# Performance work log

Hardware: AMD Instinct MI355X
Metric: run time of the kernel (lower is better)

## Reference

```python
import jax, jax.numpy as jnp
import numpy as np

N = 50000      # nodes
E = 800000     # edges (before self loops)
IN, H, OUT = 128, 64, 64
NEG_SLOPE = 0.2  # PyG GATConv leaky_relu slope


def _glorot(k, shape):
    lim = float(np.sqrt(6.0 / (shape[0] + shape[1])))
    return jax.random.uniform(k, shape, jnp.float32, -lim, lim)


def setup_inputs() -> dict:
    key = jax.random.key(0)
    ks = jax.random.split(key, 16)
    x = jax.random.normal(ks[0], (N, IN), jnp.float32)
    edge_src = jax.random.randint(ks[1], (E,), 0, N, jnp.int32)
    edge_dst = jax.random.randint(ks[2], (E,), 0, N, jnp.int32)
    dims = [(IN, H), (H, H), (H, OUT)]
    inp = {"x": x, "edge_src": edge_src, "edge_dst": edge_dst}
    i = 3
    for l, (di, do) in enumerate(dims):
        inp[f"W{l}"] = _glorot(ks[i], (di, do)); i += 1
        inp[f"as{l}"] = _glorot(ks[i], (1, do))[0]; i += 1
        inp[f"ad{l}"] = _glorot(ks[i], (1, do))[0]; i += 1
        inp[f"b{l}"] = jnp.zeros((do,), jnp.float32)
    return inp


def _gat_layer(x, W, a_src, a_dst, b, src, dst):
    # single-head GATConv (PyG semantics, self loops already in src/dst)
    h = x @ W                              # [N, do]
    s = h @ a_src                          # [N] source attention logits
    d = h @ a_dst                          # [N] dest attention logits
    e = jax.nn.leaky_relu(s[src] + d[dst], NEG_SLOPE)   # [E']
    # segment softmax over incoming edges of each destination node
    m = jax.ops.segment_max(e, dst, num_segments=N)
    w = jnp.exp(e - m[dst])
    denom = jax.ops.segment_sum(w, dst, num_segments=N)
    coef = w / (denom[dst] + 1e-16)
    out = jax.ops.segment_sum(h[src] * coef[:, None], dst, num_segments=N)
    return out + b


def reference(x, edge_src, edge_dst, W0, as0, ad0, b0, W1, as1, ad1, b1, W2, as2, ad2, b2):
    # add self loops (GATConv default add_self_loops=True)
    loop = jnp.arange(N, dtype=edge_src.dtype)
    src = jnp.concatenate([edge_src, loop])
    dst = jnp.concatenate([edge_dst, loop])
    h = jax.nn.relu(_gat_layer(x, W0, as0, ad0, b0, src, dst))
    # dropout is identity in eval mode
    h = jax.nn.relu(_gat_layer(h, W1, as1, ad1, b1, src, dst))
    return _gat_layer(h, W2, as2, ad2, b2, src, dst)
```

## Files before the change

### kernel.cpp

```cpp
#include <hip/hip_runtime.h>
#include <hip/hip_fp16.h>
#include <math.h>

#define WAVE 64
#define NEG_SLOPE 0.2f
#define BCAP 4096
#define CSTR (BCAP + 128)

typedef _Float16 half8 __attribute__((ext_vector_type(8)));
typedef float f32x4 __attribute__((ext_vector_type(4)));


template <int K, int IS_HALF>
__device__ __forceinline__ void gemm_body(
    char* smemRaw, int t, int bid,
    const void* __restrict__ Xv, const float* __restrict__ W,
    const float* __restrict__ a_s, const float* __restrict__ a_d,
    __half* __restrict__ H, float* __restrict__ S, float* __restrict__ D,
    int n) {
    constexpr int AK = K + 8;
    _Float16* Xs = (_Float16*)smemRaw;
    _Float16* Bt = Xs + 64 * AK;
    int base = bid * 64;

    {
        int row = t >> 2, q = t & 3;
        int grow = base + row;
        constexpr int CW = K / 4;
        if constexpr (IS_HALF) {
            const __half* Xh = (const __half*)Xv;
#pragma unroll
            for (int c0 = 0; c0 < CW; c0 += 8) {
                uint4 v = make_uint4(0, 0, 0, 0);
                if (grow < n) v = *(const uint4*)(Xh + (size_t)grow * K + q * CW + c0);
                *(uint4*)(Xs + row * AK + q * CW + c0) = v;
            }
        } else {
            const float* X = (const float*)Xv;
#pragma unroll
            for (int c0 = 0; c0 < CW; c0 += 8) {
                float4 v0 = make_float4(0.f, 0.f, 0.f, 0.f), v1 = v0;
                if (grow < n) {
                    v0 = *(const float4*)(X + (size_t)grow * K + q * CW + c0);
                    v1 = *(const float4*)(X + (size_t)grow * K + q * CW + c0 + 4);
                }
                _Float16 h[8] = {(_Float16)v0.x, (_Float16)v0.y, (_Float16)v0.z, (_Float16)v0.w,
                                 (_Float16)v1.x, (_Float16)v1.y, (_Float16)v1.z, (_Float16)v1.w};
                *(uint4*)(Xs + row * AK + q * CW + c0) = *(uint4*)h;
            }
        }
    }
    {
        int nn = t & 63, g = t >> 6;
        constexpr int KW = K / 4;
        _Float16 hbuf[KW];
#pragma unroll
        for (int j = 0; j < KW; ++j)
            hbuf[j] = (_Float16)W[(size_t)(g * KW + j) * 64 + nn];
#pragma unroll
        for (int j = 0; j < KW; j += 8)
            *(uint4*)(Bt + nn * AK + g * KW + j) = *(uint4*)(hbuf + j);
    }
    __syncthreads();

    int lane = t & 63;
    int wv = t >> 6;
    int m0 = wv * 16;
    int l15 = lane & 15, quad = lane >> 4;

    f32x4 acc[4] = {{0.f, 0.f, 0.f, 0.f}, {0.f, 0.f, 0.f, 0.f},
                    {0.f, 0.f, 0.f, 0.f}, {0.f, 0.f, 0.f, 0.f}};
#pragma unroll
    for (int ks = 0; ks < K; ks += 32) {
        half8 a = *(half8*)(Xs + (m0 + l15) * AK + ks + quad * 8);
#pragma unroll
        for (int cg = 0; cg < 4; ++cg) {
            half8 b = *(half8*)(Bt + (cg * 16 + l15) * AK + ks + quad * 8);
            acc[cg] = __builtin_amdgcn_mfma_f32_16x16x32_f16(a, b, acc[cg], 0, 0, 0);
        }
    }

    float as_c[4], ad_c[4];
#pragma unroll
    for (int cg = 0; cg < 4; ++cg) {
        as_c[cg] = a_s[cg * 16 + l15];
        ad_c[cg] = a_d[cg * 16 + l15];
    }
#pragma unroll
    for (int r = 0; r < 4; ++r) {
        int grow = base + m0 + quad * 4 + r;
        bool ok = grow < n;
        float ps = 0.f, pd = 0.f;
#pragma unroll
        for (int cg = 0; cg < 4; ++cg) {
            float v = acc[cg][r];
            if (ok) H[(size_t)grow * 64 + cg * 16 + l15] = __float2half(v);
            ps += v * as_c[cg];
            pd += v * ad_c[cg];
        }
        for (int o = 1; o < 16; o <<= 1) {
            ps += __shfl_xor(ps, o);
            pd += __shfl_xor(pd, o);
        }
        if (l15 == 0 && ok) { S[grow] = ps; D[grow] = pd; }
    }
}

__global__ __launch_bounds__(256) void place_gemm0_kernel(
    const int* __restrict__ src, const int* __restrict__ dst,
    int* __restrict__ gfill, int* __restrict__ binned, int e, int nb, int nchunk,
    const float* __restrict__ X, const float* __restrict__ W,
    const float* __restrict__ a_s, const float* __restrict__ a_d,
    __half* __restrict__ H, float* __restrict__ S, float* __restrict__ D, int n) {
    extern __shared__ char smem[];
    if ((int)blockIdx.x >= nchunk) {
        gemm_body<128, 0>(smem, threadIdx.x, blockIdx.x - nchunk,
                          X, W, a_s, a_d, H, S, D, n);
        return;
    }
    int* cnt = (int*)smem;
    int* bas = cnt + nb;
    for (int b = threadIdx.x; b < nb; b += 256) cnt[b] = 0;
    __syncthreads();
    int base = blockIdx.x * 4096;
#pragma unroll
    for (int k = 0; k < 16; ++k) {
        int i = base + k * 256 + threadIdx.x;
        if (i < e) atomicAdd(&cnt[dst[i] >> 7], 1);
    }
    __syncthreads();
    for (int b = threadIdx.x; b < nb; b += 256) {
        int c = cnt[b];
        bas[b] = c ? atomicAdd(&gfill[b], c) : 0;
        cnt[b] = 0;
    }
    __syncthreads();
#pragma unroll
    for (int k = 0; k < 16; ++k) {
        int i = base + k * 256 + threadIdx.x;
        if (i < e) {
            int d = dst[i];
            int bk = d >> 7;
            int r = atomicAdd(&cnt[bk], 1);
            binned[(size_t)bk * BCAP + bas[bk] + r] = ((d & 127) << 16) | src[i];
        }
    }
}

__global__ __launch_bounds__(256) void bucket_build_kernel(
    const int* __restrict__ binned, const int* __restrict__ gfill,
    int* __restrict__ csr_src, int2* __restrict__ rowse, int n) {
    __shared__ int cnt[128], off[128], pcnt[128];
    int b = blockIdx.x;
    int t = threadIdx.x;
    int nodeBase = b << 7;
    int nc = min(128, n - nodeBase);
    int ne = min(gfill[b], BCAP);
    const int* bp = binned + (size_t)b * BCAP;
    if (t < 128) { cnt[t] = 1; pcnt[t] = 1; }
    __syncthreads();
    for (int i = t; i < ne; i += 256)
        atomicAdd(&cnt[bp[i] >> 16], 1);
    __syncthreads();
    if (t < 128) off[t] = cnt[t];
    __syncthreads();
    for (int o = 1; o < 128; o <<= 1) {
        int u = (t >= o && t < 128) ? off[t - o] : 0;
        __syncthreads();
        if (t < 128) off[t] += u;
        __syncthreads();
    }
    if (t < 128) off[t] -= cnt[t];
    __syncthreads();
    int csrBase = b * CSTR;
    if (t < nc) {
        int st = csrBase + off[t];
        rowse[nodeBase + t] = make_int2(st, st + cnt[t]);
        csr_src[st] = nodeBase + t;
    }
    for (int i = t; i < ne; i += 256) {
        int p = bp[i];
        int loc = p >> 16;
        int r = atomicAdd(&pcnt[loc], 1);
        csr_src[csrBase + off[loc] + r] = p & 0xFFFF;
    }
}

template <int K, int IS_HALF>
__global__ __launch_bounds__(256) void mfma_gemm_feat_kernel(
    const void* __restrict__ Xv, const float* __restrict__ W,
    const float* __restrict__ a_s, const float* __restrict__ a_d,
    __half* __restrict__ H, float* __restrict__ S, float* __restrict__ D, int n) {
    __shared__ char smem[2 * 64 * (K + 8) * 2];
    gemm_body<K, IS_HALF>(smem, threadIdx.x, blockIdx.x, Xv, W, a_s, a_d, H, S, D, n);
}


template <int WRITE_HALF>
__global__ __launch_bounds__(256) void gat_aggregate_kernel(
    const __half* __restrict__ H, const float* __restrict__ S,
    const float* __restrict__ D, const int2* __restrict__ rowse,
    const int* __restrict__ csr_src, const float* __restrict__ bias,
    void* __restrict__ OUTp, int n, int do_relu) {
    int wid  = (blockIdx.x * blockDim.x + threadIdx.x) >> 6;
    int lane = threadIdx.x & 63;
    if (wid >= n) return;
    int eg = lane >> 3;
    int cg = lane & 7;
    int2 se = rowse[wid];
    int start = se.x, end = se.y;
    float d_i = D[wid];

    float z = 0.f;
    float acc[8] = {0.f, 0.f, 0.f, 0.f, 0.f, 0.f, 0.f, 0.f};

    for (int cb = start; cb < end; cb += WAVE) {
        int j = cb + lane;
        bool v = j < end;
        int sc = v ? csr_src[j] : 0;
        float sv = S[sc];
        float e = sv + d_i;
        e = (e > 0.f) ? e : NEG_SLOPE * e;
        float w = v ? __expf(e) : 0.f;
        z += w;

        int nch = min(WAVE, end - cb);
        int rounds = (nch + 7) >> 3;
#pragma unroll 4
        for (int r = 0; r < rounds; ++r) {
            int idx = 8 * r + eg;
            float wr = __shfl(w, idx);
            int   sr = __shfl(sc, idx);
            if (idx < nch) {
                uint4 u = *(const uint4*)(H + (size_t)sr * 64 + 8 * cg);
                float2 f0 = __half22float2(*(__half2*)&u.x);
                float2 f1 = __half22float2(*(__half2*)&u.y);
                float2 f2 = __half22float2(*(__half2*)&u.z);
                float2 f3 = __half22float2(*(__half2*)&u.w);
                acc[0] = fmaf(wr, f0.x, acc[0]);
                acc[1] = fmaf(wr, f0.y, acc[1]);
                acc[2] = fmaf(wr, f1.x, acc[2]);
                acc[3] = fmaf(wr, f1.y, acc[3]);
                acc[4] = fmaf(wr, f2.x, acc[4]);
                acc[5] = fmaf(wr, f2.y, acc[5]);
                acc[6] = fmaf(wr, f3.x, acc[6]);
                acc[7] = fmaf(wr, f3.y, acc[7]);
            }
        }
    }

    z += __shfl_xor(z, 1);
    z += __shfl_xor(z, 2);
    z += __shfl_xor(z, 4);
    for (int o = 8; o < 64; o <<= 1) {
#pragma unroll
        for (int jj = 0; jj < 8; ++jj) acc[jj] += __shfl_xor(acc[jj], o);
        z += __shfl_xor(z, o);
    }

    if (eg == 0) {
        float inv = 1.f / (z + 1e-16f);
        const float4 bv0 = *(const float4*)(bias + 8 * cg);
        const float4 bv1 = *(const float4*)(bias + 8 * cg + 4);
        float o[8];
        o[0] = acc[0] * inv + bv0.x;
        o[1] = acc[1] * inv + bv0.y;
        o[2] = acc[2] * inv + bv0.z;
        o[3] = acc[3] * inv + bv0.w;
        o[4] = acc[4] * inv + bv1.x;
        o[5] = acc[5] * inv + bv1.y;
        o[6] = acc[6] * inv + bv1.z;
        o[7] = acc[7] * inv + bv1.w;
        if (do_relu) {
#pragma unroll
            for (int jj = 0; jj < 8; ++jj) o[jj] = fmaxf(o[jj], 0.f);
        }
        if constexpr (WRITE_HALF) {
            _Float16 h[8];
#pragma unroll
            for (int jj = 0; jj < 8; ++jj) h[jj] = (_Float16)o[jj];
            *(uint4*)((__half*)OUTp + (size_t)wid * 64 + 8 * cg) = *(uint4*)h;
        } else {
            float* OUT = (float*)OUTp;
            *(float4*)(OUT + (size_t)wid * 64 + 8 * cg) = make_float4(o[0], o[1], o[2], o[3]);
            *(float4*)(OUT + (size_t)wid * 64 + 8 * cg + 4) = make_float4(o[4], o[5], o[6], o[7]);
        }
    }
}


static inline size_t align256(size_t x) { return (x + 255) & ~(size_t)255; }

extern "C" void kernel_launch(void* const* d_in, const int* in_sizes, int n_in,
                              void* d_out, int out_size, void* d_ws, size_t ws_size,
                              hipStream_t stream) {
    const float* x    = (const float*)d_in[0];
    const int*   esrc = (const int*)d_in[1];
    const int*   edst = (const int*)d_in[2];
    const int E = in_sizes[1];
    const int N = in_sizes[0] / 128;

    const float* W0 = (const float*)d_in[3];
    const float* as0 = (const float*)d_in[4];
    const float* ad0 = (const float*)d_in[5];
    const float* b0 = (const float*)d_in[6];
    const float* W1 = (const float*)d_in[7];
    const float* as1 = (const float*)d_in[8];
    const float* ad1 = (const float*)d_in[9];
    const float* b1 = (const float*)d_in[10];
    const float* W2 = (const float*)d_in[11];
    const float* as2 = (const float*)d_in[12];
    const float* ad2 = (const float*)d_in[13];
    const float* b2 = (const float*)d_in[14];

    const int NB = (N + 127) >> 7;

    char* p = (char*)d_ws;
    int*  gfill   = (int*)p;  p += align256((size_t)(NB + 1) * 4);
    int2* rowse   = (int2*)p; p += align256((size_t)N * 8);
    int*  csr_src = (int*)p;  p += align256((size_t)NB * CSTR * 4);
    int*  binned  = (int*)p;  p += align256((size_t)NB * BCAP * 4);
    __half* h16 = (__half*)p; p += align256((size_t)N * 64 * 2);
    __half* hA  = (__half*)p; p += align256((size_t)N * 64 * 2);
    __half* hB  = (__half*)p; p += align256((size_t)N * 64 * 2);
    float* sA = (float*)p; p += align256((size_t)N * 4);
    float* dA = (float*)p; p += align256((size_t)N * 4);
    float* out = (float*)d_out;

    int nchunk = (E + 4095) / 4096;
    int tile_grid = (N + 63) / 64;
    int agg_grid  = (N + 3) / 4;

    hipMemsetAsync(gfill, 0, (size_t)(NB + 1) * 4, stream);

    place_gemm0_kernel<<<nchunk + tile_grid, 256, 34816, stream>>>(
        esrc, edst, gfill, binned, E, NB, nchunk,
        x, W0, as0, ad0, h16, sA, dA, N);

    bucket_build_kernel<<<NB, 256, 0, stream>>>(binned, gfill, csr_src, rowse, N);

    gat_aggregate_kernel<1><<<agg_grid, 256, 0, stream>>>(
        h16, sA, dA, rowse, csr_src, b0, hA, N, 1);

    mfma_gemm_feat_kernel<64, 1><<<tile_grid, 256, 0, stream>>>(hA, W1, as1, ad1, h16, sA, dA, N);
    gat_aggregate_kernel<1><<<agg_grid, 256, 0, stream>>>(
        h16, sA, dA, rowse, csr_src, b1, hB, N, 1);

    mfma_gemm_feat_kernel<64, 1><<<tile_grid, 256, 0, stream>>>(hB, W2, as2, ad2, h16, sA, dA, N);
    gat_aggregate_kernel<0><<<agg_grid, 256, 0, stream>>>(
        h16, sA, dA, rowse, csr_src, b2, out, N, 0);
}
```

Measured before the change: 235.0 us.

## Split feature matrix into two 32-column halves and aggregate per half-wave

Stores the fp16 node features as two planar halves of 32 columns each. The aggregation now uses two waves per node, each gathering 64-byte rows from one half, and each edge-group lane computes its own attention weight directly instead of broadcasting weights and indices by shuffle. The aim is more waves in flight and smaller gather footprints for the irregular neighbor reads. In exchange, the attention logits, csr index and S lookups are computed twice per edge (once per half), and separate S/D buffers are added for the middle layer.

```diff
diff --git a/kernel.cpp b/kernel.cpp
--- a/kernel.cpp
+++ b/kernel.cpp
@@ -14,7 +14,8 @@
 template <int K, int IS_HALF>
 __device__ __forceinline__ void gemm_body(
     char* smemRaw, int t, int bid,
-    const void* __restrict__ Xv, const float* __restrict__ W,
+    const void* __restrict__ Xv, size_t HS,
+    const float* __restrict__ W,
     const float* __restrict__ a_s, const float* __restrict__ a_d,
     __half* __restrict__ H, float* __restrict__ S, float* __restrict__ D,
     int n) {
@@ -32,7 +33,9 @@
 #pragma unroll
             for (int c0 = 0; c0 < CW; c0 += 8) {
                 uint4 v = make_uint4(0, 0, 0, 0);
-                if (grow < n) v = *(const uint4*)(Xh + (size_t)grow * K + q * CW + c0);
+                if (grow < n)
+                    v = *(const uint4*)(Xh + (size_t)(q >> 1) * HS +
+                                        (size_t)grow * 32 + (q & 1) * 16 + c0);
                 *(uint4*)(Xs + row * AK + q * CW + c0) = v;
             }
         } else {
@@ -94,7 +97,8 @@
 #pragma unroll
         for (int cg = 0; cg < 4; ++cg) {
             float v = acc[cg][r];
-            if (ok) H[(size_t)grow * 64 + cg * 16 + l15] = __float2half(v);
+            if (ok) H[(size_t)(cg >> 1) * HS + (size_t)grow * 32 + (cg & 1) * 16 + l15] =
+                        __float2half(v);
             ps += v * as_c[cg];
             pd += v * ad_c[cg];
         }
@@ -109,13 +113,13 @@
 __global__ __launch_bounds__(256) void place_gemm0_kernel(
     const int* __restrict__ src, const int* __restrict__ dst,
     int* __restrict__ gfill, int* __restrict__ binned, int e, int nb, int nchunk,
-    const float* __restrict__ X, const float* __restrict__ W,
+    const float* __restrict__ X, size_t HS, const float* __restrict__ W,
     const float* __restrict__ a_s, const float* __restrict__ a_d,
     __half* __restrict__ H, float* __restrict__ S, float* __restrict__ D, int n) {
     extern __shared__ char smem[];
     if ((int)blockIdx.x >= nchunk) {
         gemm_body<128, 0>(smem, threadIdx.x, blockIdx.x - nchunk,
-                          X, W, a_s, a_d, H, S, D, n);
+                          X, HS, W, a_s, a_d, H, S, D, n);
         return;
     }
     int* cnt = (int*)smem;
@@ -188,102 +192,79 @@
 
 template <int K, int IS_HALF>
 __global__ __launch_bounds__(256) void mfma_gemm_feat_kernel(
-    const void* __restrict__ Xv, const float* __restrict__ W,
+    const void* __restrict__ Xv, size_t HS, const float* __restrict__ W,
     const float* __restrict__ a_s, const float* __restrict__ a_d,
     __half* __restrict__ H, float* __restrict__ S, float* __restrict__ D, int n) {
     __shared__ char smem[2 * 64 * (K + 8) * 2];
-    gemm_body<K, IS_HALF>(smem, threadIdx.x, blockIdx.x, Xv, W, a_s, a_d, H, S, D, n);
+    gemm_body<K, IS_HALF>(smem, threadIdx.x, blockIdx.x, Xv, HS, W, a_s, a_d, H, S, D, n);
 }
 
 
 template <int WRITE_HALF>
 __global__ __launch_bounds__(256) void gat_aggregate_kernel(
-    const __half* __restrict__ H, const float* __restrict__ S,
+    const __half* __restrict__ H, size_t HS, const float* __restrict__ S,
     const float* __restrict__ D, const int2* __restrict__ rowse,
-    const int* __restrict__ csr_src, const float* __restrict__ bias,
+    const int* __restrict__ csr, const float* __restrict__ bias,
     void* __restrict__ OUTp, int n, int do_relu) {
-    int wid  = (blockIdx.x * blockDim.x + threadIdx.x) >> 6;
+    int gw   = (blockIdx.x * blockDim.x + threadIdx.x) >> 6;
     int lane = threadIdx.x & 63;
-    if (wid >= n) return;
+    if (gw >= 2 * n) return;
+    int node = gw >> 1;
+    int half = gw & 1;
     int eg = lane >> 3;
     int cg = lane & 7;
-    int2 se = rowse[wid];
+    int2 se = rowse[node];
     int start = se.x, end = se.y;
-    float d_i = D[wid];
+    float d_i = D[node];
+    const __half* Hh = H + (size_t)half * HS;
 
     float z = 0.f;
-    float acc[8] = {0.f, 0.f, 0.f, 0.f, 0.f, 0.f, 0.f, 0.f};
-
-    for (int cb = start; cb < end; cb += WAVE) {
-        int j = cb + lane;
-        bool v = j < end;
-        int sc = v ? csr_src[j] : 0;
-        float sv = S[sc];
-        float e = sv + d_i;
-        e = (e > 0.f) ? e : NEG_SLOPE * e;
-        float w = v ? __expf(e) : 0.f;
-        z += w;
-
-        int nch = min(WAVE, end - cb);
-        int rounds = (nch + 7) >> 3;
+    float acc[4] = {0.f, 0.f, 0.f, 0.f};
+
 #pragma unroll 4
-        for (int r = 0; r < rounds; ++r) {
-            int idx = 8 * r + eg;
-            float wr = __shfl(w, idx);
-            int   sr = __shfl(sc, idx);
-            if (idx < nch) {
-                uint4 u = *(const uint4*)(H + (size_t)sr * 64 + 8 * cg);
-                float2 f0 = __half22float2(*(__half2*)&u.x);
-                float2 f1 = __half22float2(*(__half2*)&u.y);
-                float2 f2 = __half22float2(*(__half2*)&u.z);
-                float2 f3 = __half22float2(*(__half2*)&u.w);
-                acc[0] = fmaf(wr, f0.x, acc[0]);
-                acc[1] = fmaf(wr, f0.y, acc[1]);
-                acc[2] = fmaf(wr, f1.x, acc[2]);
-                acc[3] = fmaf(wr, f1.y, acc[3]);
-                acc[4] = fmaf(wr, f2.x, acc[4]);
-                acc[5] = fmaf(wr, f2.y, acc[5]);
-                acc[6] = fmaf(wr, f3.x, acc[6]);
-                acc[7] = fmaf(wr, f3.y, acc[7]);
-            }
-        }
-    }
-
-    z += __shfl_xor(z, 1);
-    z += __shfl_xor(z, 2);
-    z += __shfl_xor(z, 4);
+    for (int j0 = start; j0 < end; j0 += 8) {
+        int j = j0 + eg;
+        if (j < end) {
+            int sc = csr[j];
+            float e = S[sc] + d_i;
+            e = (e > 0.f) ? e : NEG_SLOPE * e;
+            float w = __expf(e);
+            uint2 u = *(const uint2*)(Hh + (size_t)sc * 32 + 4 * cg);
+            float2 f0 = __half22float2(*(__half2*)&u.x);
+            float2 f1 = __half22float2(*(__half2*)&u.y);
+            acc[0] = fmaf(w, f0.x, acc[0]);
+            acc[1] = fmaf(w, f0.y, acc[1]);
+            acc[2] = fmaf(w, f1.x, acc[2]);
+            acc[3] = fmaf(w, f1.y, acc[3]);
+            if (cg == 0) z += w;
+        }
+    }
+
     for (int o = 8; o < 64; o <<= 1) {
 #pragma unroll
-        for (int jj = 0; jj < 8; ++jj) acc[jj] += __shfl_xor(acc[jj], o);
+        for (int jj = 0; jj < 4; ++jj) acc[jj] += __shfl_xor(acc[jj], o);
         z += __shfl_xor(z, o);
     }
+    z = __shfl(z, 0);
 
     if (eg == 0) {
         float inv = 1.f / (z + 1e-16f);
-        const float4 bv0 = *(const float4*)(bias + 8 * cg);
-        const float4 bv1 = *(const float4*)(bias + 8 * cg + 4);
-        float o[8];
-        o[0] = acc[0] * inv + bv0.x;
-        o[1] = acc[1] * inv + bv0.y;
-        o[2] = acc[2] * inv + bv0.z;
-        o[3] = acc[3] * inv + bv0.w;
-        o[4] = acc[4] * inv + bv1.x;
-        o[5] = acc[5] * inv + bv1.y;
-        o[6] = acc[6] * inv + bv1.z;
-        o[7] = acc[7] * inv + bv1.w;
+        const float4 bv = *(const float4*)(bias + half * 32 + 4 * cg);
+        float o0 = acc[0] * inv + bv.x;
+        float o1 = acc[1] * inv + bv.y;
+        float o2 = acc[2] * inv + bv.z;
+        float o3 = acc[3] * inv + bv.w;
         if (do_relu) {
-#pragma unroll
-            for (int jj = 0; jj < 8; ++jj) o[jj] = fmaxf(o[jj], 0.f);
+            o0 = fmaxf(o0, 0.f); o1 = fmaxf(o1, 0.f);
+            o2 = fmaxf(o2, 0.f); o3 = fmaxf(o3, 0.f);
         }
         if constexpr (WRITE_HALF) {
-            _Float16 h[8];
-#pragma unroll
-            for (int jj = 0; jj < 8; ++jj) h[jj] = (_Float16)o[jj];
-            *(uint4*)((__half*)OUTp + (size_t)wid * 64 + 8 * cg) = *(uint4*)h;
+            _Float16 h[4] = {(_Float16)o0, (_Float16)o1, (_Float16)o2, (_Float16)o3};
+            *(uint2*)((__half*)OUTp + (size_t)half * HS + (size_t)node * 32 + 4 * cg) =
+                *(uint2*)h;
         } else {
-            float* OUT = (float*)OUTp;
-            *(float4*)(OUT + (size_t)wid * 64 + 8 * cg) = make_float4(o[0], o[1], o[2], o[3]);
-            *(float4*)(OUT + (size_t)wid * 64 + 8 * cg + 4) = make_float4(o[4], o[5], o[6], o[7]);
+            *(float4*)((float*)OUTp + (size_t)node * 64 + half * 32 + 4 * cg) =
+                make_float4(o0, o1, o2, o3);
         }
     }
 }
@@ -314,39 +295,44 @@
     const float* b2 = (const float*)d_in[14];
 
     const int NB = (N + 127) >> 7;
+    const size_t HS = (size_t)N * 32;
 
     char* p = (char*)d_ws;
-    int*  gfill   = (int*)p;  p += align256((size_t)(NB + 1) * 4);
-    int2* rowse   = (int2*)p; p += align256((size_t)N * 8);
-    int*  csr_src = (int*)p;  p += align256((size_t)NB * CSTR * 4);
-    int*  binned  = (int*)p;  p += align256((size_t)NB * BCAP * 4);
-    __half* h16 = (__half*)p; p += align256((size_t)N * 64 * 2);
-    __half* hA  = (__half*)p; p += align256((size_t)N * 64 * 2);
-    __half* hB  = (__half*)p; p += align256((size_t)N * 64 * 2);
+    int*  gfill  = (int*)p;  p += align256((size_t)(NB + 1) * 4);
+    int2* rowse  = (int2*)p; p += align256((size_t)N * 8);
+    int*  csr    = (int*)p;  p += align256((size_t)NB * CSTR * 4);
+    int*  binned = (int*)p;  p += align256((size_t)NB * BCAP * 4);
+    __half* h16  = (__half*)p; p += align256((size_t)N * 64 * 2);
+    __half* hA   = (__half*)p; p += align256((size_t)N * 64 * 2);
+    __half* hB   = (__half*)p; p += align256((size_t)N * 64 * 2);
     float* sA = (float*)p; p += align256((size_t)N * 4);
     float* dA = (float*)p; p += align256((size_t)N * 4);
+    float* sB = (float*)p; p += align256((size_t)N * 4);
+    float* dB = (float*)p; p += align256((size_t)N * 4);
     float* out = (float*)d_out;
 
     int nchunk = (E + 4095) / 4096;
     int tile_grid = (N + 63) / 64;
-    int agg_grid  = (N + 3) / 4;
+    int agg_grid  = (2 * N + 3) / 4;
 
     hipMemsetAsync(gfill, 0, (size_t)(NB + 1) * 4, stream);
 
     place_gemm0_kernel<<<nchunk + tile_grid, 256, 34816, stream>>>(
         esrc, edst, gfill, binned, E, NB, nchunk,
-        x, W0, as0, ad0, h16, sA, dA, N);
-
-    bucket_build_kernel<<<NB, 256, 0, stream>>>(binned, gfill, csr_src, rowse, N);
+        x, HS, W0, as0, ad0, h16, sA, dA, N);
+
+    bucket_build_kernel<<<NB, 256, 0, stream>>>(binned, gfill, csr, rowse, N);
 
     gat_aggregate_kernel<1><<<agg_grid, 256, 0, stream>>>(
-        h16, sA, dA, rowse, csr_src, b0, hA, N, 1);
-
-    mfma_gemm_feat_kernel<64, 1><<<tile_grid, 256, 0, stream>>>(hA, W1, as1, ad1, h16, sA, dA, N);
+        h16, HS, sA, dA, rowse, csr, b0, hA, N, 1);
+
+    mfma_gemm_feat_kernel<64, 1><<<tile_grid, 256, 0, stream>>>(
+        hA, HS, W1, as1, ad1, h16, sB, dB, N);
     gat_aggregate_kernel<1><<<agg_grid, 256, 0, stream>>>(
-        h16, sA, dA, rowse, csr_src, b1, hB, N, 1);
-
-    mfma_gemm_feat_kernel<64, 1><<<tile_grid, 256, 0, stream>>>(hB, W2, as2, ad2, h16, sA, dA, N);
+        h16, HS, sB, dB, rowse, csr, b1, hB, N, 1);
+
+    mfma_gemm_feat_kernel<64, 1><<<tile_grid, 256, 0, stream>>>(
+        hB, HS, W2, as2, ad2, h16, sA, dA, N);
     gat_aggregate_kernel<0><<<agg_grid, 256, 0, stream>>>(
-        h16, sA, dA, rowse, csr_src, b2, out, N, 0);
-}
+        h16, HS, sA, dA, rowse, csr, b2, out, N, 0);
+}
```

New measurement: 281.7 us. 19.9% more time.
